# Kernel optimization log

Hardware: AMD Instinct MI355X
Metric: run time of the kernel (lower is better)

Reference implementation:

```python
import jax, jax.numpy as jnp
import numpy as np

N_NODES, N_EDGES, CH, FEAT = 20000, 320000, 256, 118


def setup_inputs() -> dict:
    key = jax.random.key(0)
    ks = jax.random.split(key, 8)
    x = jax.random.uniform(ks[0], (N_NODES, FEAT), dtype=jnp.float32)
    edge_index = jax.random.randint(ks[1], (2, N_EDGES), 0, N_NODES, dtype=jnp.int64)
    s = 0.05
    W_embed = jax.random.normal(ks[2], (FEAT, CH), dtype=jnp.float32) * s
    b_embed = jnp.zeros((CH,), jnp.float32)
    W1 = jax.random.normal(ks[3], (CH, CH), dtype=jnp.float32) * s
    b1 = jnp.zeros((CH,), jnp.float32)
    W2 = jax.random.normal(ks[4], (CH, CH), dtype=jnp.float32) * s
    b2 = jnp.zeros((CH,), jnp.float32)
    return {"x": x, "edge_index": edge_index, "W_embed": W_embed, "b_embed": b_embed,
            "W1": W1, "b1": b1, "W2": W2, "b2": b2}


def reference(x, edge_index, W_embed, b_embed, W1, b1, W2, b2):
    n = x.shape[0]
    # node embedding: Linear(118 -> C)
    h = x @ W_embed + b_embed  # [N, C]
    src, dst = edge_index[0], edge_index[1]
    # message: gather x_j per edge, dense1 + exact GELU (dropout = identity in eval)
    msg = jax.nn.gelu(h[src] @ W1 + b1, approximate=False)  # [E, C]
    # mean aggregation into destination nodes
    agg = jax.ops.segment_sum(msg, dst, num_segments=n)  # [N, C]
    cnt = jax.ops.segment_sum(jnp.ones((msg.shape[0],), msg.dtype), dst, num_segments=n)
    agg = agg / jnp.maximum(cnt, 1.0)[:, None]
    # update: dense2 + exact GELU
    out = jax.nn.gelu(agg @ W2 + b2, approximate=False)  # [N, C]
    # final mean over channel dim
    return out.mean(axis=1)  # [N]
```

## Files before the change

kernel.cpp:

```cpp
#include <hip/hip_runtime.h>
#include <math.h>

#define N_NODES 20000
#define N_EDGES 320000
#define CH      256
#define FEAT    118
#define CAP     48

typedef float    f32x4 __attribute__((ext_vector_type(4)));
typedef short    s16x8 __attribute__((ext_vector_type(8)));
typedef _Float16 f16x4 __attribute__((ext_vector_type(4)));
typedef _Float16 f16x8 __attribute__((ext_vector_type(8)));
typedef unsigned short u16;

union Frag  { s16x8 v; u16 u[8]; };
union FragH { f16x8 v; _Float16 h[8]; };

__device__ __forceinline__ float gelu_exact(float x) {
    return 0.5f * x * (1.0f + erff(x * 0.70710678118654752f));
}
__device__ __forceinline__ u16 f2bf(float f) {
    unsigned u = __float_as_uint(f);
    u = (u + 0x7FFFu + ((u >> 16) & 1u)) >> 16;
    return (u16)u;
}
__device__ __forceinline__ float bf2f(u16 h) { return __uint_as_float(((unsigned)h) << 16); }

__global__ __launch_bounds__(256) void prep(const float* __restrict__ x,
                                            const int* __restrict__ ei,
                                            const float* __restrict__ We,
                                            const float* __restrict__ be,
                                            const float* __restrict__ W1,
                                            const float* __restrict__ b1,
                                            const float* __restrict__ W2,
                                            u16* __restrict__ xh, u16* __restrict__ xl,
                                            int* __restrict__ cnt, int* __restrict__ bins,
                                            _Float16* __restrict__ w2h, _Float16* __restrict__ w2l,
                                            u16* __restrict__ wch, u16* __restrict__ wcl,
                                            float* __restrict__ bc) {
    const int b = blockIdx.x, tid = threadIdx.x;
    if (b < 1250) {
        __shared__ float xs[16][132];
        {
            int r = tid >> 4, ci = tid & 15;
            const float* xrow = x + (size_t)(b * 16 + r) * FEAT;
            #pragma unroll
            for (int it = 0; it < 8; it++) {
                int col = ci + it * 16;
                xs[r][col] = (col < FEAT) ? xrow[col] : 0.0f;
            }
        }
        __syncthreads();
        int lane = tid & 63, ks = tid >> 6;
        int row = lane & 15, k0 = ks * 32 + (lane >> 4) * 8;
        Frag hi, lo;
        #pragma unroll
        for (int j = 0; j < 8; j++) {
            float v = xs[row][k0 + j];
            u16 h = f2bf(v);
            hi.u[j] = h; lo.u[j] = f2bf(v - bf2f(h));
        }
        size_t fid = (size_t)b * 256 + tid;
        ((s16x8*)xh)[fid] = hi.v;
        ((s16x8*)xl)[fid] = lo.v;
    } else if (b < 2500) {
        int e = (b - 1250) * 256 + tid;
        int s = ei[e];
        int d = ei[N_EDGES + e];
        int p = atomicAdd(&cnt[d], 1);
        if (p < CAP) bins[(size_t)d * CAP + p] = s;
    } else if (b < 2532) {
        int fid = (b - 2500) * 256 + tid;
        int lane = fid & 63, ks = (fid >> 6) & 7, nt = fid >> 9;
        int n = nt * 16 + (lane & 15);
        int k0 = ks * 32 + (lane >> 4) * 8;
        FragH hi, lo;
        #pragma unroll
        for (int j = 0; j < 8; j++) {
            float v = W2[(size_t)(k0 + j) * 256 + n];
            _Float16 h = (_Float16)v;
            hi.h[j] = h;
            lo.h[j] = (_Float16)((v - (float)h) * 4096.0f);
        }
        ((f16x8*)w2h)[fid] = hi.v;
        ((f16x8*)w2l)[fid] = lo.v;
    } else {
        int f = b - 2532;
        int n = tid;
        if (f < 128) {
            float acc = 0.0f;
            if (f < FEAT) {
                const float* wr = We + (size_t)f * 256;
                #pragma unroll 8
                for (int c = 0; c < 256; c++) acc += wr[c] * W1[(size_t)c * 256 + n];
            }
            int nt = n >> 4, lm = n & 15, ks = f >> 5, q = (f >> 3) & 3, j = f & 7;
            size_t idx = (((size_t)nt * 4 + ks) * 64 + q * 16 + lm) * 8 + j;
            u16 h = f2bf(acc);
            wch[idx] = h;
            wcl[idx] = f2bf(acc - bf2f(h));
        } else {
            float acc = b1[n];
            #pragma unroll 8
            for (int c = 0; c < 256; c++) acc += be[c] * W1[(size_t)c * 256 + n];
            bc[n] = acc;
        }
    }
}

__global__ __launch_bounds__(256) void gemm_main(const u16* __restrict__ Ah_, const u16* __restrict__ Al_,
                                                 const u16* __restrict__ Bh_, const u16* __restrict__ Bl_,
                                                 const float* __restrict__ bias,
                                                 _Float16* __restrict__ Mout) {
    __shared__ _Float16 Ls[16][256];
    const int tid = threadIdx.x, wave = tid >> 6, lane = tid & 63;
    const int quad = lane >> 4, lm = lane & 15;
    const int mt = blockIdx.x, nt0 = wave * 4;
    const s16x8* Ah = (const s16x8*)Ah_; const s16x8* Al = (const s16x8*)Al_;
    const s16x8* Bh = (const s16x8*)Bh_; const s16x8* Bl = (const s16x8*)Bl_;
    f32x4 acc[4] = {f32x4{0,0,0,0}, f32x4{0,0,0,0}, f32x4{0,0,0,0}, f32x4{0,0,0,0}};
    #pragma unroll
    for (int ks = 0; ks < 4; ks++) {
        s16x8 a_h = Ah[((size_t)mt * 4 + ks) * 64 + lane];
        s16x8 a_l = Al[((size_t)mt * 4 + ks) * 64 + lane];
        #pragma unroll
        for (int t = 0; t < 4; t++) {
            s16x8 bh = Bh[((size_t)(nt0 + t) * 4 + ks) * 64 + lane];
            s16x8 bl = Bl[((size_t)(nt0 + t) * 4 + ks) * 64 + lane];
            acc[t] = __builtin_amdgcn_mfma_f32_16x16x32_bf16(a_h, bh, acc[t], 0, 0, 0);
            acc[t] = __builtin_amdgcn_mfma_f32_16x16x32_bf16(a_l, bh, acc[t], 0, 0, 0);
            acc[t] = __builtin_amdgcn_mfma_f32_16x16x32_bf16(a_h, bl, acc[t], 0, 0, 0);
        }
    }
    #pragma unroll
    for (int t = 0; t < 4; t++) {
        float bn = bias[(nt0 + t) * 16 + lm];
        #pragma unroll
        for (int r = 0; r < 4; r++)
            Ls[quad * 4 + r][(nt0 + t) * 16 + lm] = (_Float16)gelu_exact(acc[t][r] + bn);
    }
    __syncthreads();
    s16x8* dst = (s16x8*)Mout + (size_t)mt * 512;
    const s16x8* src = (const s16x8*)&Ls[0][0];
    dst[tid]       = src[tid];
    dst[256 + tid] = src[256 + tid];
}

__global__ __launch_bounds__(256) void aggregate(const _Float16* __restrict__ M,
                                                 const int* __restrict__ cnt,
                                                 const int* __restrict__ bins,
                                                 _Float16* __restrict__ aggf) {
    int node = (blockIdx.x * 256 + threadIdx.x) >> 6;
    int lane = threadIdx.x & 63;
    int c = cnt[node];
    int cc = min(c, CAP);
    int myid = (lane < CAP) ? bins[(size_t)node * CAP + lane] : 0;
    float a0 = 0.f, a1 = 0.f, a2 = 0.f, a3 = 0.f;
    for (int j = 0; j < cc; j += 8) {
        f16x4 v[8];
        #pragma unroll
        for (int u = 0; u < 8; u++) {
            int s = __shfl(myid, min(j + u, cc - 1), 64);
            v[u] = *(const f16x4*)(M + (size_t)s * CH + lane * 4);
        }
        #pragma unroll
        for (int u = 0; u < 8; u++) {
            if (j + u < cc) {
                a0 += (float)v[u].x; a1 += (float)v[u].y;
                a2 += (float)v[u].z; a3 += (float)v[u].w;
            }
        }
    }
    float inv = 1.0f / (float)max(c, 1);
    f16x4 o;
    o.x = (_Float16)(a0 * inv); o.y = (_Float16)(a1 * inv);
    o.z = (_Float16)(a2 * inv); o.w = (_Float16)(a3 * inv);
    int mt = node >> 4, lm = node & 15;
    int ks = lane >> 3, quad = (lane & 7) >> 1, j0 = (lane & 1) * 4;
    size_t base = (((size_t)mt * 8 + ks) * 64 + quad * 16 + lm) * 8 + j0;
    *(f16x4*)(aggf + base) = o;
}

__global__ __launch_bounds__(256) void gemm_mean(const _Float16* __restrict__ Af_,
                                                 const _Float16* __restrict__ Bh_, const _Float16* __restrict__ Bl_,
                                                 const float* __restrict__ bias,
                                                 float* __restrict__ out) {
    __shared__ float part[4][32];
    const int tid = threadIdx.x, wave = tid >> 6, lane = tid & 63;
    const int quad = lane >> 4, lm = lane & 15;
    const int mt0 = blockIdx.x * 2, nt0 = wave * 4;
    const f16x8* Af = (const f16x8*)Af_;
    const f16x8* Bh = (const f16x8*)Bh_; const f16x8* Bl = (const f16x8*)Bl_;
    f32x4 acch[2][4], accl[2][4];
    #pragma unroll
    for (int mi = 0; mi < 2; mi++)
        #pragma unroll
        for (int t = 0; t < 4; t++) {
            acch[mi][t] = f32x4{0.f, 0.f, 0.f, 0.f};
            accl[mi][t] = f32x4{0.f, 0.f, 0.f, 0.f};
        }
    #pragma unroll
    for (int ks = 0; ks < 8; ks++) {
        f16x8 a0 = Af[((size_t)(mt0 + 0) * 8 + ks) * 64 + lane];
        f16x8 a1 = Af[((size_t)(mt0 + 1) * 8 + ks) * 64 + lane];
        #pragma unroll
        for (int t = 0; t < 4; t++) {
            f16x8 bh = Bh[((size_t)(nt0 + t) * 8 + ks) * 64 + lane];
            f16x8 bl = Bl[((size_t)(nt0 + t) * 8 + ks) * 64 + lane];
            acch[0][t] = __builtin_amdgcn_mfma_f32_16x16x32_f16(a0, bh, acch[0][t], 0, 0, 0);
            accl[0][t] = __builtin_amdgcn_mfma_f32_16x16x32_f16(a0, bl, accl[0][t], 0, 0, 0);
            acch[1][t] = __builtin_amdgcn_mfma_f32_16x16x32_f16(a1, bh, acch[1][t], 0, 0, 0);
            accl[1][t] = __builtin_amdgcn_mfma_f32_16x16x32_f16(a1, bl, accl[1][t], 0, 0, 0);
        }
    }
    float p[2][4] = {{0.f,0.f,0.f,0.f},{0.f,0.f,0.f,0.f}};
    #pragma unroll
    for (int t = 0; t < 4; t++) {
        float bn = bias[(nt0 + t) * 16 + lm];
        #pragma unroll
        for (int mi = 0; mi < 2; mi++)
            #pragma unroll
            for (int r = 0; r < 4; r++)
                p[mi][r] += gelu_exact(acch[mi][t][r] + accl[mi][t][r] * (1.0f / 4096.0f) + bn);
    }
    #pragma unroll
    for (int off = 1; off < 16; off <<= 1)
        #pragma unroll
        for (int mi = 0; mi < 2; mi++)
            #pragma unroll
            for (int r = 0; r < 4; r++)
                p[mi][r] += __shfl_xor(p[mi][r], off, 64);
    if (lm == 0)
        #pragma unroll
        for (int mi = 0; mi < 2; mi++)
            #pragma unroll
            for (int r = 0; r < 4; r++)
                part[wave][mi * 16 + quad * 4 + r] = p[mi][r];
    __syncthreads();
    if (tid < 32) {
        float s = part[0][tid] + part[1][tid] + part[2][tid] + part[3][tid];
        out[blockIdx.x * 32 + tid] = s * (1.0f / 256.0f);
    }
}

extern "C" void kernel_launch(void* const* d_in, const int* in_sizes, int n_in,
                              void* d_out, int out_size, void* d_ws, size_t ws_size,
                              hipStream_t stream) {
    const float* x  = (const float*)d_in[0];
    const int*   ei = (const int*)d_in[1];
    const float* We = (const float*)d_in[2];
    const float* be = (const float*)d_in[3];
    const float* W1 = (const float*)d_in[4];
    const float* b1 = (const float*)d_in[5];
    const float* W2 = (const float*)d_in[6];
    const float* b2 = (const float*)d_in[7];
    float* out = (float*)d_out;

    char* ws = (char*)d_ws;
    size_t off = 0;
    u16* xh = (u16*)(ws + off);
    _Float16* aggf = (_Float16*)(ws + off);
    off += 5120000;
    u16* xl = (u16*)(ws + off); off += 5120000;
    _Float16* M = (_Float16*)(ws + off); off += 10240000;
    u16* wch = (u16*)(ws + off); off += 65536;
    u16* wcl = (u16*)(ws + off); off += 65536;
    _Float16* w2h = (_Float16*)(ws + off); off += 131072;
    _Float16* w2l = (_Float16*)(ws + off); off += 131072;
    float* bc = (float*)(ws + off); off += 1024;
    int* cnt  = (int*)(ws + off); off += N_NODES * 4;
    int* bins = (int*)(ws + off); off += (size_t)N_NODES * CAP * 4;

    hipMemsetAsync(cnt, 0, N_NODES * sizeof(int), stream);
    prep<<<2661, 256, 0, stream>>>(x, ei, We, be, W1, b1, W2,
                                   xh, xl, cnt, bins, w2h, w2l, wch, wcl, bc);
    gemm_main<<<N_NODES / 16, 256, 0, stream>>>(xh, xl, wch, wcl, bc, M);
    aggregate<<<N_NODES / 4, 256, 0, stream>>>(M, cnt, bins, aggf);
    gemm_mean<<<N_NODES / 32, 256, 0, stream>>>(aggf, w2h, w2l, b2, out);
}
```

Baseline: 152.3 us.

## Split aggregation across channel slices with edge-parallel lanes and shuffle reduction

Each node's aggregation is now spread over 8 blocks, each covering a 32-channel slice. Within a wave, 16 edges are loaded in parallel as 16-byte f16x8 vectors, and the partial sums are combined with xor shuffles. The goal is more memory-level parallelism and fewer serial gather iterations per node. In exchange, the cnt and bins reads are repeated 8 times, the launch grid grows, and the shuffle reduction adds work.

```diff
diff --git a/kernel.cpp b/kernel.cpp
--- a/kernel.cpp
+++ b/kernel.cpp
@@ -150,35 +150,36 @@
                                                  const int* __restrict__ cnt,
                                                  const int* __restrict__ bins,
                                                  _Float16* __restrict__ aggf) {
-    int node = (blockIdx.x * 256 + threadIdx.x) >> 6;
-    int lane = threadIdx.x & 63;
+    const int sl = blockIdx.x & 7;
+    const int wave = threadIdx.x >> 6, lane = threadIdx.x & 63;
+    const int node = (blockIdx.x >> 3) * 4 + wave;
+    const int esub = lane >> 2, c4 = lane & 3;
     int c = cnt[node];
     int cc = min(c, CAP);
-    int myid = (lane < CAP) ? bins[(size_t)node * CAP + lane] : 0;
-    float a0 = 0.f, a1 = 0.f, a2 = 0.f, a3 = 0.f;
-    for (int j = 0; j < cc; j += 8) {
-        f16x4 v[8];
-        #pragma unroll
-        for (int u = 0; u < 8; u++) {
-            int s = __shfl(myid, min(j + u, cc - 1), 64);
-            v[u] = *(const f16x4*)(M + (size_t)s * CH + lane * 4);
-        }
-        #pragma unroll
-        for (int u = 0; u < 8; u++) {
-            if (j + u < cc) {
-                a0 += (float)v[u].x; a1 += (float)v[u].y;
-                a2 += (float)v[u].z; a3 += (float)v[u].w;
-            }
-        }
-    }
-    float inv = 1.0f / (float)max(c, 1);
-    f16x4 o;
-    o.x = (_Float16)(a0 * inv); o.y = (_Float16)(a1 * inv);
-    o.z = (_Float16)(a2 * inv); o.w = (_Float16)(a3 * inv);
-    int mt = node >> 4, lm = node & 15;
-    int ks = lane >> 3, quad = (lane & 7) >> 1, j0 = (lane & 1) * 4;
-    size_t base = (((size_t)mt * 8 + ks) * 64 + quad * 16 + lm) * 8 + j0;
-    *(f16x4*)(aggf + base) = o;
+    int myid = (lane < cc) ? bins[(size_t)node * CAP + lane] : 0;
+    float a[8] = {0.f, 0.f, 0.f, 0.f, 0.f, 0.f, 0.f, 0.f};
+    for (int j = 0; j < cc; j += 16) {
+        int e = min(j + esub, cc - 1);
+        int s = __shfl(myid, e, 64);
+        f16x8 v = *(const f16x8*)(M + (size_t)s * CH + sl * 32 + c4 * 8);
+        if (j + esub < cc) {
+            #pragma unroll
+            for (int q = 0; q < 8; q++) a[q] += (float)v[q];
+        }
+    }
+    #pragma unroll
+    for (int off = 4; off < 64; off <<= 1)
+        #pragma unroll
+        for (int q = 0; q < 8; q++) a[q] += __shfl_xor(a[q], off, 64);
+    if (esub == 0) {
+        float inv = 1.0f / (float)max(c, 1);
+        FragH o;
+        #pragma unroll
+        for (int q = 0; q < 8; q++) o.h[q] = (_Float16)(a[q] * inv);
+        int mt = node >> 4, lm = node & 15;
+        size_t base = (((size_t)mt * 8 + sl) * 64 + c4 * 16 + lm) * 8;
+        *(f16x8*)(aggf + base) = o.v;
+    }
 }
 
 __global__ __launch_bounds__(256) void gemm_mean(const _Float16* __restrict__ Af_,
@@ -275,6 +276,6 @@
     prep<<<2661, 256, 0, stream>>>(x, ei, We, be, W1, b1, W2,
                                    xh, xl, cnt, bins, w2h, w2l, wch, wcl, bc);
     gemm_main<<<N_NODES / 16, 256, 0, stream>>>(xh, xl, wch, wcl, bc, M);
-    aggregate<<<N_NODES / 4, 256, 0, stream>>>(M, cnt, bins, aggf);
+    aggregate<<<(N_NODES / 4) * 8, 256, 0, stream>>>(M, cnt, bins, aggf);
     gemm_mean<<<N_NODES / 32, 256, 0, stream>>>(aggf, w2h, w2l, b2, out);
 }
```

Result: slower. 187.9 us (+23.3%).
